# Optimization experiments

Measured on AMD Instinct MI355X. Metric: run time of the kernel, lower is better.

## Reference

```python
import jax, jax.numpy as jnp
import numpy as np

N = 20000   # nodes
E = 200000  # edges
D = 32      # inp_dim == out_dim == emb_dim
R = 100     # num_rel
EPS = 1e-5  # BatchNorm1d default eps


def setup_inputs() -> dict:
    key = jax.random.key(0)
    ks = jax.random.split(key, 5)
    h = jax.random.normal(ks[0], (N, D), dtype=jnp.float32)
    # xavier_uniform-ish scale for [R, D, D] relation weights
    weight = jax.random.normal(ks[1], (R, D, D), dtype=jnp.float32) * (1.0 / np.sqrt(D))
    gamma = jnp.ones((D,), dtype=jnp.float32)
    beta = jnp.zeros((D,), dtype=jnp.float32)
    src = jax.random.randint(ks[2], (E,), 0, N, dtype=jnp.int32)
    dst = jax.random.randint(ks[3], (E,), 0, N, dtype=jnp.int32)
    etype = jax.random.randint(ks[4], (E,), 0, R, dtype=jnp.int32)
    return {"h": h, "weight": weight, "gamma": gamma, "beta": beta,
            "src": src, "dst": dst, "etype": etype}


def reference(h, weight, gamma, beta, src, dst, etype):
    # per-edge relation-weight gather: [E, D, D]
    w_e = weight[etype]
    # per-edge bmm (src feature row-vector @ relation matrix) + relu: [E, D]
    msg = jax.nn.relu(jnp.einsum('ed,edo->eo', h[src], w_e))
    # BatchNorm1d in training mode: batch stats over the edge dimension
    mu = jnp.mean(msg, axis=0)
    var = jnp.mean(jnp.square(msg - mu), axis=0)  # biased variance
    msg = (msg - mu) * jax.lax.rsqrt(var + EPS) * gamma + beta
    # segment-mean reduce of messages into destination nodes: [N, D]
    ssum = jax.ops.segment_sum(msg, dst, num_segments=N)
    cnt = jax.ops.segment_sum(jnp.ones((E,), msg.dtype), dst, num_segments=N)
    return ssum / jnp.maximum(cnt, 1.0)[:, None]
```

## Files before the change

kernel.cpp:

```cpp
#include <hip/hip_runtime.h>

#define D 32
#define EPS 1e-5f
#define TPB 256
#define NB 256

__global__ void hist2_kernel(const int* __restrict__ etype, int E, int R, int chunk,
                             int* __restrict__ blockHistT)
{
    __shared__ int lh[1024];
    for (int i = threadIdx.x; i < R; i += TPB) lh[i] = 0;
    __syncthreads();
    const int lo = blockIdx.x * chunk, hi = min(E, lo + chunk);
    for (int e = lo + threadIdx.x; e < hi; e += TPB)
        atomicAdd(&lh[etype[e]], 1);
    __syncthreads();
    for (int r = threadIdx.x; r < R; r += TPB)
        blockHistT[r * NB + blockIdx.x] = lh[r];
}

__global__ void scan2_kernel(int* __restrict__ blockHistT, int R,
                             int* __restrict__ rel_start,
                             int* __restrict__ task_rel, int* __restrict__ task_start,
                             int* __restrict__ n_tasks)
{
    __shared__ int tot[1024];
    __shared__ int s_start[1025];
    __shared__ int s_tbase[1024];
    const int r = threadIdx.x;
    if (r < R) {
        int acc = 0;
        int* p = blockHistT + r * NB;
        for (int b = 0; b < NB; ++b) { int v = p[b]; p[b] = acc; acc += v; }
        tot[r] = acc;
    }
    __syncthreads();
    if (threadIdx.x == 0) {
        int acc = 0, tb = 0;
        for (int rr = 0; rr < R; ++rr) {
            s_start[rr] = acc; s_tbase[rr] = tb;
            acc += tot[rr];
            tb  += (tot[rr] + TPB - 1) / TPB;
        }
        s_start[R] = acc;
        rel_start[R] = acc;
        *n_tasks = tb;
    }
    __syncthreads();
    if (r < R) {
        const int st = s_start[r];
        rel_start[r] = st;
        const int nb = (tot[r] + TPB - 1) / TPB;
        const int tb = s_tbase[r];
        for (int b = 0; b < nb; ++b) {
            task_rel[tb + b]   = r;
            task_start[tb + b] = st + b * TPB;
        }
    }
}

__global__ void scatter2_kernel(const int* __restrict__ src, const int* __restrict__ dst,
                                const int* __restrict__ etype, int E, int R, int chunk,
                                const int* __restrict__ blockHistT,
                                const int* __restrict__ rel_start,
                                int* __restrict__ ssrc, int* __restrict__ sdst)
{
    __shared__ int cur[1024];
    for (int r = threadIdx.x; r < R; r += TPB)
        cur[r] = rel_start[r] + blockHistT[r * NB + blockIdx.x];
    __syncthreads();
    const int lo = blockIdx.x * chunk, hi = min(E, lo + chunk);
    for (int e = lo + threadIdx.x; e < hi; e += TPB) {
        const int p = atomicAdd(&cur[etype[e]], 1);
        ssrc[p] = src[e];
        sdst[p] = dst[e];
    }
}

__global__ __launch_bounds__(TPB)
void rgcn_main(const float* __restrict__ h, const float* __restrict__ W,
               const int* __restrict__ rel_start,
               const int* __restrict__ task_rel, const int* __restrict__ task_start,
               const int* __restrict__ n_tasks_p,
               const int* __restrict__ ssrc, const int* __restrict__ sdst,
               float* __restrict__ out,
               float* __restrict__ stat_sum, float* __restrict__ stat_sq,
               float* __restrict__ cnt)
{
    __shared__ float s_tile[TPB * 33];
    __shared__ int   s_src[TPB];
    __shared__ int   s_dst[TPB];
    __shared__ float s_aux[2 * TPB];

    const int task = blockIdx.x;
    if (task >= *n_tasks_p) return;
    const int r      = task_rel[task];
    const int start  = task_start[task];
    const int relEnd = rel_start[r + 1];
    const int nE     = min(TPB, relEnd - start);
    const int tid    = threadIdx.x;

    if (tid < nE) {
        s_src[tid] = ssrc[start + tid];
        s_dst[tid] = sdst[start + tid];
    }
    __syncthreads();

    for (int i = tid; i < nE * 8; i += TPB) {
        const int row = i >> 3, seg = i & 7;
        const float4 v = *(const float4*)(h + (size_t)s_src[row] * D + seg * 4);
        float* p = &s_tile[row * 33 + seg * 4];
        p[0] = v.x; p[1] = v.y; p[2] = v.z; p[3] = v.w;
    }
    __syncthreads();

    const float* Wr = W + (size_t)__builtin_amdgcn_readfirstlane(r) * (D * D);

    float acc[D];
#pragma unroll
    for (int o = 0; o < D; ++o) acc[o] = 0.f;

    if (tid < nE) {
#pragma unroll 4
        for (int d = 0; d < D; ++d) {
            const float hd = s_tile[tid * 33 + d];
#pragma unroll
            for (int o = 0; o < D; ++o)
                acc[o] = fmaf(hd, Wr[d * D + o], acc[o]);
        }
#pragma unroll
        for (int o = 0; o < D; ++o) acc[o] = fmaxf(acc[o], 0.f);
        atomicAdd(&cnt[s_dst[tid]], 1.0f);
    }
    __syncthreads();

    if (tid < nE) {
#pragma unroll
        for (int o = 0; o < D; ++o) s_tile[tid * 33 + o] = acc[o];
    }
    __syncthreads();

    float ps = 0.f, pq = 0.f;
    for (int i = tid; i < nE * D; i += TPB) {
        const int row = i >> 5, o = i & 31;
        const float v = s_tile[row * 33 + o];
        atomicAdd(&out[(size_t)s_dst[row] * D + o], v);
        ps += v; pq += v * v;
    }
    s_aux[tid]       = ps;
    s_aux[TPB + tid] = pq;
    __syncthreads();
    if (tid < D) {
        float ss = 0.f, sq = 0.f;
#pragma unroll
        for (int c = 0; c < TPB / D; ++c) {
            ss += s_aux[c * D + tid];
            sq += s_aux[TPB + c * D + tid];
        }
        atomicAdd(&stat_sum[tid], ss);
        atomicAdd(&stat_sq[tid], sq);
    }
}

__global__ void finalize_kernel(float* __restrict__ out, const float* __restrict__ cnt,
                                const float* __restrict__ stat_sum,
                                const float* __restrict__ stat_sq,
                                const float* __restrict__ gamma,
                                const float* __restrict__ beta,
                                float invE, int total)
{
    const int i = blockIdx.x * TPB + threadIdx.x;
    if (i >= total) return;
    const int o    = i & 31;
    const int node = i >> 5;
    const float mu  = stat_sum[o] * invE;
    const float var = fmaxf(stat_sq[o] * invE - mu * mu, 0.f);
    const float is  = rsqrtf(var + EPS);
    const float sc  = gamma[o] * is;
    const float sh  = fmaf(-mu, sc, beta[o]);
    const float c   = cnt[node];
    out[i] = fmaf(out[i], sc, sh * c) / fmaxf(c, 1.0f);
}

extern "C" void kernel_launch(void* const* d_in, const int* in_sizes, int n_in,
                              void* d_out, int out_size, void* d_ws, size_t ws_size,
                              hipStream_t stream)
{
    const float* h     = (const float*)d_in[0];
    const float* W     = (const float*)d_in[1];
    const float* gamma = (const float*)d_in[2];
    const float* beta  = (const float*)d_in[3];
    const int*   src   = (const int*)d_in[4];
    const int*   dst   = (const int*)d_in[5];
    const int*   etype = (const int*)d_in[6];
    float* out = (float*)d_out;

    const int E = in_sizes[4];
    const int N = in_sizes[0] / D;
    const int R = in_sizes[1] / (D * D);
    const int T = R + (E + TPB - 1) / TPB;
    const int chunk = (E + NB - 1) / NB;

    float* stat_sum  = (float*)d_ws;
    float* stat_sq   = stat_sum + D;
    float* cnt       = stat_sq + D;
    int*   rel_start = (int*)(cnt + N);
    int*   n_tasks   = rel_start + R + 1;
    int*   task_rel  = n_tasks + 1;
    int*   task_start= task_rel + T;
    int*   blockHistT= task_start + T;
    int*   ssrc      = blockHistT + R * NB;
    int*   sdst      = ssrc + E;

    hipMemsetAsync(d_ws, 0, sizeof(float) * (size_t)(2 * D + N), stream);
    hipMemsetAsync(d_out, 0, sizeof(float) * (size_t)out_size, stream);

    hist2_kernel<<<NB, TPB, 0, stream>>>(etype, E, R, chunk, blockHistT);
    scan2_kernel<<<1, TPB, 0, stream>>>(blockHistT, R, rel_start,
                                        task_rel, task_start, n_tasks);
    scatter2_kernel<<<NB, TPB, 0, stream>>>(src, dst, etype, E, R, chunk,
                                            blockHistT, rel_start, ssrc, sdst);
    rgcn_main<<<T, TPB, 0, stream>>>(h, W, rel_start, task_rel, task_start,
                                     n_tasks, ssrc, sdst, out,
                                     stat_sum, stat_sq, cnt);
    finalize_kernel<<<(N * D + TPB - 1) / TPB, TPB, 0, stream>>>(
        out, cnt, stat_sum, stat_sq, gamma, beta, 1.0f / (float)E, N * D);
}
```

Measured before the change: 152.7 us.

## Replace atomic scatter-add with dst-sorted message buffer and segmented gather reduce

Adds a new pipeline that counting-sorts edges by destination as well as by relation. Each edge's message is written into a contiguous destination-ordered buffer, and a per-node kernel then sums its messages without float atomics. Batch-norm statistics move to a separate pass over that buffer. The aim is to remove the heavy global float atomicAdd traffic on the output, at the cost of an extra E×D workspace buffer, a serial single-block scan, and extra kernel launches. The new path runs only when the workspace is large enough; otherwise the old path is used.

After: 211.4 us. +38.4%, slower.

```diff
diff --git a/kernel.cpp b/kernel.cpp
--- a/kernel.cpp
+++ b/kernel.cpp
@@ -4,6 +4,212 @@
 #define EPS 1e-5f
 #define TPB 256
 #define NB 256
+#define NB2 1024
+
+
+__global__ void k1_hist(const int* __restrict__ etype, const int* __restrict__ dst,
+                        int E, int R,
+                        int* __restrict__ relHist, int* __restrict__ cnt)
+{
+    __shared__ int lh[1024];
+    for (int i = threadIdx.x; i < R; i += TPB) lh[i] = 0;
+    __syncthreads();
+    for (int e = blockIdx.x * TPB + threadIdx.x; e < E; e += gridDim.x * TPB) {
+        atomicAdd(&lh[etype[e]], 1);
+        atomicAdd(&cnt[dst[e]], 1);
+    }
+    __syncthreads();
+    for (int r = threadIdx.x; r < R; r += TPB)
+        if (lh[r]) atomicAdd(&relHist[r], lh[r]);
+}
+
+__global__ __launch_bounds__(1024)
+void k2_scan(const int* __restrict__ relHist, int R, int E, int N,
+             int* __restrict__ rel_start, int* __restrict__ cursor_rel,
+             int* __restrict__ task_rel, int* __restrict__ task_start,
+             int* __restrict__ n_tasks,
+             const int* __restrict__ cnt,
+             int* __restrict__ dst_base, int* __restrict__ cursor_dst)
+{
+    const int t = threadIdx.x;
+    __shared__ int sb[1024];
+    __shared__ int s_start[1025];
+    __shared__ int s_tbase[1024];
+
+    if (t == 0) {
+        int acc = 0, tb = 0;
+        for (int r = 0; r < R; ++r) {
+            s_start[r] = acc; s_tbase[r] = tb;
+            const int v = relHist[r];
+            acc += v;
+            tb  += (v + TPB - 1) / TPB;
+        }
+        s_start[R] = acc;
+        *n_tasks = tb;
+    }
+    __syncthreads();
+    if (t < R) {
+        const int st = s_start[t];
+        rel_start[t]  = st;
+        cursor_rel[t] = st;
+        const int tot = s_start[t + 1] - st;
+        const int nb  = (tot + TPB - 1) / TPB;
+        const int tb  = s_tbase[t];
+        for (int b = 0; b < nb; ++b) {
+            task_rel[tb + b]   = t;
+            task_start[tb + b] = st + b * TPB;
+        }
+    }
+    if (t == 0) rel_start[R] = s_start[R];
+
+    const int chunk = (N + 1023) >> 10;
+    const int lo = t * chunk, hi = min(N, lo + chunk);
+    int part = 0;
+    for (int i = lo; i < hi; ++i) part += cnt[i];
+    sb[t] = part;
+    __syncthreads();
+    for (int off = 1; off < 1024; off <<= 1) {
+        const int v = (t >= off) ? sb[t - off] : 0;
+        __syncthreads();
+        sb[t] += v;
+        __syncthreads();
+    }
+    int base = sb[t] - part;
+    for (int i = lo; i < hi; ++i) {
+        dst_base[i]   = base;
+        cursor_dst[i] = base;
+        base += cnt[i];
+    }
+    if (t == 0) dst_base[N] = E;
+}
+
+__global__ void k3_scatter(const int* __restrict__ src, const int* __restrict__ dst,
+                           const int* __restrict__ etype, int E, int R, int chunk,
+                           int* __restrict__ cursor_rel, int* __restrict__ cursor_dst,
+                           int* __restrict__ ssrc, int* __restrict__ tpos)
+{
+    __shared__ int lh[1024];
+    __shared__ int lcur[1024];
+    for (int r = threadIdx.x; r < R; r += TPB) lh[r] = 0;
+    __syncthreads();
+    const int lo = blockIdx.x * chunk, hi = min(E, lo + chunk);
+    for (int e = lo + threadIdx.x; e < hi; e += TPB)
+        atomicAdd(&lh[etype[e]], 1);
+    __syncthreads();
+    for (int r = threadIdx.x; r < R; r += TPB)
+        lcur[r] = lh[r] ? atomicAdd(&cursor_rel[r], lh[r]) : 0;
+    __syncthreads();
+    for (int e = lo + threadIdx.x; e < hi; e += TPB) {
+        const int p = atomicAdd(&lcur[etype[e]], 1);
+        ssrc[p] = src[e];
+        tpos[p] = atomicAdd(&cursor_dst[dst[e]], 1);
+    }
+}
+
+__global__ __launch_bounds__(TPB)
+void k4_compute(const float* __restrict__ h, const float* __restrict__ W,
+                const int* __restrict__ rel_start,
+                const int* __restrict__ task_rel, const int* __restrict__ task_start,
+                const int* __restrict__ n_tasks_p,
+                const int* __restrict__ ssrc, const int* __restrict__ tpos,
+                float* __restrict__ msg)
+{
+    const int task = blockIdx.x;
+    if (task >= *n_tasks_p) return;
+    const int r      = task_rel[task];
+    const int start  = task_start[task];
+    const int relEnd = rel_start[r + 1];
+    const int e      = start + threadIdx.x;
+    if (e >= relEnd) return;
+
+    const float* Wr = W + (size_t)__builtin_amdgcn_readfirstlane(r) * (D * D);
+
+    const int s  = ssrc[e];
+    const int tp = tpos[e];
+    float acc[D];
+#pragma unroll
+    for (int o = 0; o < D; ++o) acc[o] = 0.f;
+    const float4* hp = (const float4*)(h + (size_t)s * D);
+#pragma unroll 4
+    for (int c = 0; c < D / 4; ++c) {
+        const float4 hv = hp[c];
+#pragma unroll
+        for (int j = 0; j < 4; ++j) {
+            const float hd = (j == 0) ? hv.x : (j == 1) ? hv.y : (j == 2) ? hv.z : hv.w;
+            const int d = c * 4 + j;
+#pragma unroll
+            for (int o = 0; o < D; ++o)
+                acc[o] = fmaf(hd, Wr[d * D + o], acc[o]);
+        }
+    }
+    float4* mp = (float4*)(msg + (size_t)tp * D);
+#pragma unroll
+    for (int c = 0; c < D / 4; ++c) {
+        float4 v;
+        v.x = fmaxf(acc[4 * c],     0.f);
+        v.y = fmaxf(acc[4 * c + 1], 0.f);
+        v.z = fmaxf(acc[4 * c + 2], 0.f);
+        v.w = fmaxf(acc[4 * c + 3], 0.f);
+        mp[c] = v;
+    }
+}
+
+__global__ __launch_bounds__(TPB)
+void k4b_stats(const float* __restrict__ msg, int E,
+               float* __restrict__ stat_sum, float* __restrict__ stat_sq)
+{
+    __shared__ float s_aux[2 * TPB];
+    const int tid = threadIdx.x;
+    const int o   = tid & (D - 1);
+    const int rpb = TPB / D;
+    float ps = 0.f, pq = 0.f;
+    for (int p = blockIdx.x * rpb + (tid >> 5); p < E; p += gridDim.x * rpb) {
+        const float v = msg[(size_t)p * D + o];
+        ps += v; pq += v * v;
+    }
+    s_aux[tid]       = ps;
+    s_aux[TPB + tid] = pq;
+    __syncthreads();
+    if (tid < D) {
+        float ss = 0.f, sq = 0.f;
+#pragma unroll
+        for (int c = 0; c < TPB / D; ++c) {
+            ss += s_aux[c * D + tid];
+            sq += s_aux[TPB + c * D + tid];
+        }
+        atomicAdd(&stat_sum[tid], ss);
+        atomicAdd(&stat_sq[tid], sq);
+    }
+}
+
+__global__ __launch_bounds__(TPB)
+void k5_reduce(const float* __restrict__ msg,
+               const int* __restrict__ dst_base,
+               const float* __restrict__ stat_sum, const float* __restrict__ stat_sq,
+               const float* __restrict__ gamma, const float* __restrict__ beta,
+               float invE, int N, float* __restrict__ out)
+{
+    __shared__ float s_sc[D], s_sh[D];
+    const int tid = threadIdx.x;
+    if (tid < D) {
+        const float mu  = stat_sum[tid] * invE;
+        const float var = fmaxf(stat_sq[tid] * invE - mu * mu, 0.f);
+        const float is  = rsqrtf(var + EPS);
+        const float sc  = gamma[tid] * is;
+        s_sc[tid] = sc;
+        s_sh[tid] = fmaf(-mu, sc, beta[tid]);
+    }
+    __syncthreads();
+    const int o    = tid & (D - 1);
+    const int node = blockIdx.x * (TPB / D) + (tid >> 5);
+    if (node >= N) return;
+    const int b0 = dst_base[node], b1 = dst_base[node + 1];
+    float v = 0.f;
+    for (int p = b0; p < b1; ++p) v += msg[(size_t)p * D + o];
+    const float c = (float)(b1 - b0);
+    out[(size_t)node * D + o] = fmaf(v, s_sc[o], s_sh[o] * c) / fmaxf(c, 1.0f);
+}
+
 
 __global__ void hist2_kernel(const int* __restrict__ etype, int E, int R, int chunk,
                              int* __restrict__ blockHistT)
@@ -201,6 +407,57 @@
     const int T = R + (E + TPB - 1) / TPB;
     const int chunk = (E + NB - 1) / NB;
 
+    const size_t o_stat_sum   = 0;
+    const size_t o_stat_sq    = o_stat_sum + D;
+    const size_t o_relHist    = o_stat_sq + D;
+    const size_t o_cursor_rel = o_relHist + R;
+    const size_t o_n_tasks    = o_cursor_rel + R;
+    const size_t o_cnt        = o_n_tasks + 1;
+    const size_t zwords       = o_cnt + (size_t)N;
+    const size_t o_rel_start  = zwords;
+    const size_t o_task_rel   = o_rel_start + R + 1;
+    const size_t o_task_start = o_task_rel + T;
+    const size_t o_dst_base   = o_task_start + T;
+    const size_t o_cursor_dst = o_dst_base + N + 1;
+    const size_t o_ssrc       = o_cursor_dst + N;
+    const size_t o_tpos       = o_ssrc + (size_t)E;
+    const size_t o_msg        = (o_tpos + (size_t)E + 3) & ~(size_t)3;
+    const size_t total_words  = o_msg + (size_t)E * D;
+
+    if (ws_size >= total_words * 4) {
+        float* stat_sum   = (float*)d_ws + o_stat_sum;
+        float* stat_sq    = (float*)d_ws + o_stat_sq;
+        int*   relHist    = (int*)d_ws + o_relHist;
+        int*   cursor_rel = (int*)d_ws + o_cursor_rel;
+        int*   n_tasks    = (int*)d_ws + o_n_tasks;
+        int*   cnt        = (int*)d_ws + o_cnt;
+        int*   rel_start  = (int*)d_ws + o_rel_start;
+        int*   task_rel   = (int*)d_ws + o_task_rel;
+        int*   task_start = (int*)d_ws + o_task_start;
+        int*   dst_base   = (int*)d_ws + o_dst_base;
+        int*   cursor_dst = (int*)d_ws + o_cursor_dst;
+        int*   ssrc       = (int*)d_ws + o_ssrc;
+        int*   tpos       = (int*)d_ws + o_tpos;
+        float* msg        = (float*)d_ws + o_msg;
+
+        hipMemsetAsync(d_ws, 0, zwords * 4, stream);
+
+        k1_hist<<<NB, TPB, 0, stream>>>(etype, dst, E, R, relHist, cnt);
+        k2_scan<<<1, 1024, 0, stream>>>(relHist, R, E, N,
+                                        rel_start, cursor_rel,
+                                        task_rel, task_start, n_tasks,
+                                        cnt, dst_base, cursor_dst);
+        k3_scatter<<<NB, TPB, 0, stream>>>(src, dst, etype, E, R, chunk,
+                                           cursor_rel, cursor_dst, ssrc, tpos);
+        k4_compute<<<T, TPB, 0, stream>>>(h, W, rel_start, task_rel, task_start,
+                                          n_tasks, ssrc, tpos, msg);
+        k4b_stats<<<NB2, TPB, 0, stream>>>(msg, E, stat_sum, stat_sq);
+        k5_reduce<<<(N + TPB / D - 1) / (TPB / D), TPB, 0, stream>>>(
+            msg, dst_base, stat_sum, stat_sq, gamma, beta,
+            1.0f / (float)E, N, out);
+        return;
+    }
+
     float* stat_sum  = (float*)d_ws;
     float* stat_sq   = stat_sum + D;
     float* cnt       = stat_sq + D;
```

## Sort edges by destination and pre-reduce segments before scattering atomics

Applied to the files above, without the earlier changes.

Adds a new pipeline that counting-sorts edges by destination node instead of by relation. Each block computes per-edge messages with weights gathered from global memory by edge type, then sums runs of equal destination in shared memory so that one atomic is issued per segment rather than per edge. The separate output memset and float count atomics are replaced by zeroing inside the histogram kernel and reading degrees from the prefix-sum array. The trade-off is uncoalesced per-lane weight loads for mixed relations, a single-block scan over 20000 nodes, and serial segment loops. The old path is kept as a fallback when the workspace is too small.

Result: slower. 261.2 us (+71.1%).

```diff
diff --git a/kernel.cpp b/kernel.cpp
--- a/kernel.cpp
+++ b/kernel.cpp
@@ -4,6 +4,182 @@
 #define EPS 1e-5f
 #define TPB 256
 #define NB 256
+
+
+__global__ void g1_hist(const int* __restrict__ dst, int E, int N,
+                        float* __restrict__ out, int* __restrict__ cnt)
+{
+    const int gid = blockIdx.x * TPB + threadIdx.x;
+    const int stride = gridDim.x * TPB;
+    for (int i = gid; i < N * D; i += stride) out[i] = 0.f;
+    for (int e = gid; e < E; e += stride) atomicAdd(&cnt[dst[e]], 1);
+}
+
+__global__ __launch_bounds__(1024)
+void g2_scan(const int* __restrict__ cnt, int N, int E,
+             int* __restrict__ dst_base, int* __restrict__ cursor_dst)
+{
+    const int t = threadIdx.x;
+    __shared__ int sb[1024];
+    const int chunk = (N + 1023) >> 10;
+    const int lo = t * chunk, hi = min(N, lo + chunk);
+    int part = 0;
+    for (int i = lo; i < hi; ++i) part += cnt[i];
+    sb[t] = part;
+    __syncthreads();
+    for (int off = 1; off < 1024; off <<= 1) {
+        const int v = (t >= off) ? sb[t - off] : 0;
+        __syncthreads();
+        sb[t] += v;
+        __syncthreads();
+    }
+    int base = sb[t] - part;
+    for (int i = lo; i < hi; ++i) {
+        dst_base[i]   = base;
+        cursor_dst[i] = base;
+        base += cnt[i];
+    }
+    if (t == 0) dst_base[N] = E;
+}
+
+__global__ void g3_scatter(const int* __restrict__ src, const int* __restrict__ dst,
+                           const int* __restrict__ etype, int E,
+                           int* __restrict__ cursor_dst,
+                           int* __restrict__ ssrc, int* __restrict__ sdst,
+                           int* __restrict__ setype)
+{
+    const int gid = blockIdx.x * TPB + threadIdx.x;
+    const int stride = gridDim.x * TPB;
+    for (int e = gid; e < E; e += stride) {
+        const int dnode = dst[e];
+        const int p = atomicAdd(&cursor_dst[dnode], 1);
+        ssrc[p]   = src[e];
+        sdst[p]   = dnode;
+        setype[p] = etype[e];
+    }
+}
+
+__global__ __launch_bounds__(TPB)
+void g4_main(const float* __restrict__ h, const float* __restrict__ W,
+             const int* __restrict__ ssrc, const int* __restrict__ sdst,
+             const int* __restrict__ setype, int E,
+             float* __restrict__ out,
+             float* __restrict__ stat_sum, float* __restrict__ stat_sq)
+{
+    __shared__ float s_tile[TPB * 33];
+    __shared__ int   s_dst[TPB];
+    __shared__ int   s_flag[TPB];
+    __shared__ int   s_segstart[TPB];
+    __shared__ float s_aux[2 * TPB];
+    __shared__ int   s_nseg;
+
+    const int tid   = threadIdx.x;
+    const int start = blockIdx.x * TPB;
+    const int nE    = min(TPB, E - start);
+    const int p     = start + tid;
+
+    if (tid == 0) s_nseg = 0;
+    if (tid < nE) s_dst[tid] = sdst[p];
+    __syncthreads();
+
+    if (tid < nE) {
+        const int et = setype[p];
+        const int s  = ssrc[p];
+        const float* Wr = W + (size_t)et * (D * D);
+
+        float hbuf[D];
+        const float4* hp = (const float4*)(h + (size_t)s * D);
+#pragma unroll
+        for (int c = 0; c < D / 4; ++c) {
+            const float4 hv = hp[c];
+            hbuf[4 * c]     = hv.x; hbuf[4 * c + 1] = hv.y;
+            hbuf[4 * c + 2] = hv.z; hbuf[4 * c + 3] = hv.w;
+        }
+
+        float acc[D];
+#pragma unroll
+        for (int o = 0; o < D; ++o) acc[o] = 0.f;
+
+        const float4* wp = (const float4*)Wr;
+#pragma unroll 4
+        for (int d = 0; d < D; ++d) {
+            const float hd = hbuf[d];
+#pragma unroll
+            for (int c = 0; c < D / 4; ++c) {
+                const float4 wv = wp[d * (D / 4) + c];
+                acc[4 * c]     = fmaf(hd, wv.x, acc[4 * c]);
+                acc[4 * c + 1] = fmaf(hd, wv.y, acc[4 * c + 1]);
+                acc[4 * c + 2] = fmaf(hd, wv.z, acc[4 * c + 2]);
+                acc[4 * c + 3] = fmaf(hd, wv.w, acc[4 * c + 3]);
+            }
+        }
+#pragma unroll
+        for (int o = 0; o < D; ++o)
+            s_tile[tid * 33 + o] = fmaxf(acc[o], 0.f);
+        s_flag[tid] = (tid == 0) || (s_dst[tid] != s_dst[tid - 1]);
+    }
+    __syncthreads();
+
+    if (tid < nE && s_flag[tid]) {
+        const int si = atomicAdd(&s_nseg, 1);
+        s_segstart[si] = tid;
+    }
+
+    float ps = 0.f, pq = 0.f;
+    for (int i = tid; i < nE * D; i += TPB) {
+        const int row = i >> 5, o = i & 31;
+        const float v = s_tile[row * 33 + o];
+        ps += v; pq += v * v;
+    }
+    s_aux[tid]       = ps;
+    s_aux[TPB + tid] = pq;
+    __syncthreads();
+
+    if (tid < D) {
+        float ss = 0.f, sq = 0.f;
+#pragma unroll
+        for (int c = 0; c < TPB / D; ++c) {
+            ss += s_aux[c * D + tid];
+            sq += s_aux[TPB + c * D + tid];
+        }
+        atomicAdd(&stat_sum[tid], ss);
+        atomicAdd(&stat_sq[tid], sq);
+    }
+
+    const int o = tid & (D - 1);
+    const int nseg = s_nseg;
+    for (int si = tid >> 5; si < nseg; si += TPB / D) {
+        const int st   = s_segstart[si];
+        const int node = s_dst[st];
+        float sum = 0.f;
+        for (int row = st; row < nE; ++row) {
+            if (row > st && s_flag[row]) break;
+            sum += s_tile[row * 33 + o];
+        }
+        atomicAdd(&out[(size_t)node * D + o], sum);
+    }
+}
+
+__global__ void g5_final(float* __restrict__ out, const int* __restrict__ dst_base,
+                         const float* __restrict__ stat_sum,
+                         const float* __restrict__ stat_sq,
+                         const float* __restrict__ gamma,
+                         const float* __restrict__ beta,
+                         float invE, int N)
+{
+    const int i = blockIdx.x * TPB + threadIdx.x;
+    if (i >= N * D) return;
+    const int o    = i & 31;
+    const int node = i >> 5;
+    const float mu  = stat_sum[o] * invE;
+    const float var = fmaxf(stat_sq[o] * invE - mu * mu, 0.f);
+    const float is  = rsqrtf(var + EPS);
+    const float sc  = gamma[o] * is;
+    const float sh  = fmaf(-mu, sc, beta[o]);
+    const float c   = (float)(dst_base[node + 1] - dst_base[node]);
+    out[i] = fmaf(out[i], sc, sh * c) / fmaxf(c, 1.0f);
+}
+
 
 __global__ void hist2_kernel(const int* __restrict__ etype, int E, int R, int chunk,
                              int* __restrict__ blockHistT)
@@ -198,13 +374,49 @@
     const int E = in_sizes[4];
     const int N = in_sizes[0] / D;
     const int R = in_sizes[1] / (D * D);
+
+    const size_t o_stat_sum   = 0;
+    const size_t o_stat_sq    = o_stat_sum + D;
+    const size_t o_cnt        = o_stat_sq + D;
+    const size_t zwords       = o_cnt + (size_t)N;
+    const size_t o_dst_base   = zwords;
+    const size_t o_cursor_dst = o_dst_base + N + 1;
+    const size_t o_ssrc       = o_cursor_dst + N;
+    const size_t o_sdst       = o_ssrc + (size_t)E;
+    const size_t o_setype     = o_sdst + (size_t)E;
+    const size_t total_words  = o_setype + (size_t)E;
+
+    if (ws_size >= total_words * 4) {
+        float* stat_sum   = (float*)d_ws + o_stat_sum;
+        float* stat_sq    = (float*)d_ws + o_stat_sq;
+        int*   cnt        = (int*)d_ws + o_cnt;
+        int*   dst_base   = (int*)d_ws + o_dst_base;
+        int*   cursor_dst = (int*)d_ws + o_cursor_dst;
+        int*   ssrc       = (int*)d_ws + o_ssrc;
+        int*   sdst       = (int*)d_ws + o_sdst;
+        int*   setype     = (int*)d_ws + o_setype;
+
+        hipMemsetAsync(d_ws, 0, zwords * 4, stream);
+
+        g1_hist<<<NB, TPB, 0, stream>>>(dst, E, N, out, cnt);
+        g2_scan<<<1, 1024, 0, stream>>>(cnt, N, E, dst_base, cursor_dst);
+        g3_scatter<<<NB, TPB, 0, stream>>>(src, dst, etype, E,
+                                           cursor_dst, ssrc, sdst, setype);
+        g4_main<<<(E + TPB - 1) / TPB, TPB, 0, stream>>>(
+            h, W, ssrc, sdst, setype, E, out, stat_sum, stat_sq);
+        g5_final<<<(N * D + TPB - 1) / TPB, TPB, 0, stream>>>(
+            out, dst_base, stat_sum, stat_sq, gamma, beta,
+            1.0f / (float)E, N);
+        return;
+    }
+
     const int T = R + (E + TPB - 1) / TPB;
     const int chunk = (E + NB - 1) / NB;
 
     float* stat_sum  = (float*)d_ws;
     float* stat_sq   = stat_sum + D;
-    float* cnt       = stat_sq + D;
-    int*   rel_start = (int*)(cnt + N);
+    float* cntf      = stat_sq + D;
+    int*   rel_start = (int*)(cntf + N);
     int*   n_tasks   = rel_start + R + 1;
     int*   task_rel  = n_tasks + 1;
     int*   task_start= task_rel + T;
@@ -222,7 +434,7 @@
                                             blockHistT, rel_start, ssrc, sdst);
     rgcn_main<<<T, TPB, 0, stream>>>(h, W, rel_start, task_rel, task_start,
                                      n_tasks, ssrc, sdst, out,
-                                     stat_sum, stat_sq, cnt);
+                                     stat_sum, stat_sq, cntf);
     finalize_kernel<<<(N * D + TPB - 1) / TPB, TPB, 0, stream>>>(
-        out, cnt, stat_sum, stat_sq, gamma, beta, 1.0f / (float)E, N * D);
-}
+        out, cntf, stat_sum, stat_sq, gamma, beta, 1.0f / (float)E, N * D);
+}
```
